# Optimization experiments

Measured on AMD Instinct MI355X. Metric: run time of the kernel, lower is better.

Reference implementation:

```python
import jax, jax.numpy as jnp
import numpy as np

N = 131072
K = 27
FIN = 3
FOUT = 32
EPS = 1e-5


def _bn(h, gamma, beta, mean, var):
    return (h - mean) * jax.lax.rsqrt(var + EPS) * gamma + beta


def setup_inputs() -> dict:
    key = jax.random.key(0)
    ks = jax.random.split(key, 8)
    return {
        "x_feats": jax.random.normal(ks[0], (N, FIN), jnp.float32),
        "z_feats": jax.random.normal(ks[1], (N, FIN), jnp.float32),
        "nbr_idx": jax.random.randint(ks[2], (N, K), 0, N, jnp.int32),
        "w1": jax.random.normal(ks[3], (K, FIN, FOUT), jnp.float32) * 0.2,
        "bn1_gamma": jnp.ones((FOUT,), jnp.float32),
        "bn1_beta": jnp.zeros((FOUT,), jnp.float32),
        "bn1_mean": jax.random.normal(ks[4], (FOUT,), jnp.float32) * 0.1,
        "bn1_var": jax.random.uniform(ks[5], (FOUT,), jnp.float32, 0.5, 1.5),
        "w2": jax.random.normal(ks[6], (K, FOUT, FOUT), jnp.float32) * 0.1,
        "mlp_w": jax.random.normal(ks[7], (FIN, FOUT), jnp.float32) * 0.3,
        "mlp_b": jnp.zeros((FOUT,), jnp.float32),
        "mlp_gamma": jnp.ones((FOUT,), jnp.float32),
        "mlp_beta": jnp.zeros((FOUT,), jnp.float32),
        "mlp_mean": jnp.zeros((FOUT,), jnp.float32),
        "mlp_var": jnp.ones((FOUT,), jnp.float32),
    }


def reference(x_feats, z_feats, nbr_idx, w1, bn1_gamma, bn1_beta, bn1_mean,
              bn1_var, w2, mlp_w, mlp_b, mlp_gamma, mlp_beta, mlp_mean,
              mlp_var):
    # --- voxel branch: sparse conv (gather-GEMM) -> BN -> SiLU -> sparse conv
    g1 = x_feats[nbr_idx]                       # [N, K, FIN] irregular gather
    h = jnp.einsum('nkf,kfo->no', g1, w1)       # [N, FOUT]
    h = jax.nn.silu(_bn(h, bn1_gamma, bn1_beta, bn1_mean, bn1_var))
    g2 = h[nbr_idx]                             # [N, K, FOUT] irregular gather
    x_out = jnp.einsum('nkf,kfo->no', g2, w2)   # [N, FOUT]

    # --- point branch: SharedMLP = Linear -> BN -> ReLU
    z = z_feats @ mlp_w + mlp_b
    z = jax.nn.relu(_bn(z, mlp_gamma, mlp_beta, mlp_mean, mlp_var))

    # --- mixed_mix: fuse voxel and point features additively
    fused = x_out + z
    return (fused, fused)
```

## Files before the change

### kernel.cpp

```cpp
#include <hip/hip_runtime.h>
#include <math.h>

#define NN 131072
#define KK 27
#define FIN 3
#define FOUT 32
#define EPS 1e-5f

typedef _Float16 f16;
typedef __attribute__((ext_vector_type(8))) _Float16 f16x8;
typedef __attribute__((ext_vector_type(16))) float f32x16;

__global__ __launch_bounds__(256) void pack_w2_kernel(
    const float* __restrict__ w2, f16* __restrict__ w2p)
{
    const int t = blockIdx.x * 256 + threadIdx.x;
    if (t >= KK * 2 * 64 * 8) return;
    const int k    = t >> 10;
    const int rem  = t & 1023;
    const int half = rem >> 9;
    const int l    = (rem >> 3) & 63;
    const int j    = rem & 7;
    const int krow = half * 16 + ((l >> 5) << 3) + j;
    const int n    = l & 31;
    w2p[t] = (f16)w2[k * (FOUT * FOUT) + krow * FOUT + n];
}

__global__ __launch_bounds__(256) void conv1_kernel(
    const float* __restrict__ x_feats,
    const int*   __restrict__ nbr_idx,
    const float* __restrict__ w1,
    const float* __restrict__ g1,  const float* __restrict__ b1,
    const float* __restrict__ m1,  const float* __restrict__ v1,
    f16* __restrict__ h_out)
{
    const int n = blockIdx.x * 256 + threadIdx.x;

    int idxs[KK];
    const int* nb = nbr_idx + (size_t)n * KK;
#pragma unroll
    for (int k = 0; k < KK; ++k) idxs[k] = nb[k];

    float acc[FOUT];
#pragma unroll
    for (int o = 0; o < FOUT; ++o) acc[o] = 0.f;

#pragma unroll
    for (int c = 0; c < 3; ++c) {
        float xs[9][3];
#pragma unroll
        for (int q = 0; q < 9; ++q) {
            const float* xr = x_feats + (size_t)idxs[c * 9 + q] * FIN;
            xs[q][0] = xr[0]; xs[q][1] = xr[1]; xs[q][2] = xr[2];
        }
#pragma unroll
        for (int q = 0; q < 9; ++q) {
            const float* w = w1 + (c * 9 + q) * (FIN * FOUT);
#pragma unroll
            for (int o = 0; o < FOUT; ++o) {
                float a = acc[o];
                a = fmaf(xs[q][0], w[o],            a);
                a = fmaf(xs[q][1], w[FOUT + o],     a);
                a = fmaf(xs[q][2], w[2 * FOUT + o], a);
                acc[o] = a;
            }
        }
    }

    f16* hr = h_out + (size_t)n * FOUT;
#pragma unroll
    for (int g = 0; g < 4; ++g) {
        f16x8 hv;
#pragma unroll
        for (int j = 0; j < 8; ++j) {
            const int o = g * 8 + j;
            const float sc = g1[o] * rsqrtf(v1[o] + EPS);
            float v = (acc[o] - m1[o]) * sc + b1[o];
            v = v / (1.f + __expf(-v));
            hv[j] = (f16)v;
        }
        *(f16x8*)(hr + g * 8) = hv;
    }
}

__global__ __launch_bounds__(256) void conv2_mfma_kernel(
    const f16*   __restrict__ h,
    const int*   __restrict__ nbr_idx,
    const f16*   __restrict__ w2p,
    const float* __restrict__ z_feats,
    const float* __restrict__ mlp_w,
    const float* __restrict__ mlp_b,
    const float* __restrict__ mg, const float* __restrict__ mbe,
    const float* __restrict__ mm, const float* __restrict__ mv,
    float* __restrict__ out)
{
    const int lane = threadIdx.x & 63;
    const int wave = threadIdx.x >> 6;
    const int base = (blockIdx.x * 4 + wave) * 32;
    const int row  = lane & 31;
    const int hi   = lane >> 5;

    int idxs[KK];
    const int* nb = nbr_idx + (size_t)(base + row) * KK;
#pragma unroll
    for (int k = 0; k < KK; ++k) idxs[k] = nb[k];

    f32x16 acc = {};

    const f16x8* bp = (const f16x8*)w2p;
#pragma unroll 3
    for (int k = 0; k < KK; ++k) {
        const f16* hr = h + (size_t)idxs[k] * FOUT + hi * 8;
        const f16x8 a1 = *(const f16x8*)hr;
        const f16x8 a2 = *(const f16x8*)(hr + 16);
        const f16x8 b1 = bp[k * 128 + lane];
        const f16x8 b2 = bp[k * 128 + 64 + lane];
        acc = __builtin_amdgcn_mfma_f32_32x32x16_f16(a1, b1, acc, 0, 0, 0);
        acc = __builtin_amdgcn_mfma_f32_32x32x16_f16(a2, b2, acc, 0, 0, 0);
    }

    const int n0 = lane & 31;
    const float wc0 = mlp_w[n0];
    const float wc1 = mlp_w[FOUT + n0];
    const float wc2 = mlp_w[2 * FOUT + n0];
    const float sc  = mg[n0] * rsqrtf(mv[n0] + EPS);
    const float bi  = mlp_b[n0];
    const float mmv = mm[n0];
    const float mbv = mbe[n0];

#pragma unroll
    for (int r = 0; r < 16; ++r) {
        const int m    = (r & 3) + ((r >> 2) << 3) + (hi << 2);
        const int node = base + m;
        const float* zr = z_feats + (size_t)node * FIN;
        float z = bi;
        z = fmaf(zr[0], wc0, z);
        z = fmaf(zr[1], wc1, z);
        z = fmaf(zr[2], wc2, z);
        z = (z - mmv) * sc + mbv;
        z = fmaxf(z, 0.f);
        const float v = acc[r] + z;
        out[(size_t)node * FOUT + n0] = v;
        out[(size_t)NN * FOUT + (size_t)node * FOUT + n0] = v;
    }
}

extern "C" void kernel_launch(void* const* d_in, const int* in_sizes, int n_in,
                              void* d_out, int out_size, void* d_ws, size_t ws_size,
                              hipStream_t stream) {
    const float* x_feats = (const float*)d_in[0];
    const float* z_feats = (const float*)d_in[1];
    const int*   nbr_idx = (const int*)d_in[2];
    const float* w1      = (const float*)d_in[3];
    const float* bn1_g   = (const float*)d_in[4];
    const float* bn1_b   = (const float*)d_in[5];
    const float* bn1_m   = (const float*)d_in[6];
    const float* bn1_v   = (const float*)d_in[7];
    const float* w2      = (const float*)d_in[8];
    const float* mlp_w   = (const float*)d_in[9];
    const float* mlp_b   = (const float*)d_in[10];
    const float* mlp_g   = (const float*)d_in[11];
    const float* mlp_be  = (const float*)d_in[12];
    const float* mlp_m   = (const float*)d_in[13];
    const float* mlp_v   = (const float*)d_in[14];

    f16* h   = (f16*)d_ws;
    f16* w2p = (f16*)((char*)d_ws + (size_t)8 * 1024 * 1024);
    float* out = (float*)d_out;

    pack_w2_kernel<<<(KK * 1024 + 255) / 256, 256, 0, stream>>>(w2, w2p);
    conv1_kernel<<<NN / 256, 256, 0, stream>>>(x_feats, nbr_idx, w1,
                                               bn1_g, bn1_b, bn1_m, bn1_v, h);
    conv2_mfma_kernel<<<NN / 128, 256, 0, stream>>>(h, nbr_idx, w2p, z_feats,
                                                    mlp_w, mlp_b, mlp_g, mlp_be,
                                                    mlp_m, mlp_v, out);
}
```

Before: 167.5 us.

## Split conv1 outputs across waves and conv2 neighbor range across wave pairs

conv1 now assigns each wave an 8-channel output slice of the same 64 nodes, so each thread keeps 8 accumulators instead of 32 and the grid has four times as many threads. conv2 splits the 27 neighbor offsets (padded to 28 with zero weights) across two waves per 32-node tile and reduces the partial MFMA accumulators through LDS. Both changes aim to raise parallelism and latency hiding for the irregular gathers. In exchange, conv1 re-gathers each node's neighbor features four times, and conv2 adds a block-wide barrier, an LDS exchange and one padded MFMA step per wave.

```diff
diff --git a/kernel.cpp b/kernel.cpp
--- a/kernel.cpp
+++ b/kernel.cpp
@@ -3,6 +3,7 @@
 
 #define NN 131072
 #define KK 27
+#define KP 28
 #define FIN 3
 #define FOUT 32
 #define EPS 1e-5f
@@ -15,7 +16,7 @@
     const float* __restrict__ w2, f16* __restrict__ w2p)
 {
     const int t = blockIdx.x * 256 + threadIdx.x;
-    if (t >= KK * 2 * 64 * 8) return;
+    if (t >= KP * 2 * 64 * 8) return;
     const int k    = t >> 10;
     const int rem  = t & 1023;
     const int half = rem >> 9;
@@ -23,7 +24,7 @@
     const int j    = rem & 7;
     const int krow = half * 16 + ((l >> 5) << 3) + j;
     const int n    = l & 31;
-    w2p[t] = (f16)w2[k * (FOUT * FOUT) + krow * FOUT + n];
+    w2p[t] = (k < KK) ? (f16)w2[k * (FOUT * FOUT) + krow * FOUT + n] : (f16)0.f;
 }
 
 __global__ __launch_bounds__(256) void conv1_kernel(
@@ -34,30 +35,32 @@
     const float* __restrict__ m1,  const float* __restrict__ v1,
     f16* __restrict__ h_out)
 {
-    const int n = blockIdx.x * 256 + threadIdx.x;
+    const int ln = threadIdx.x & 63;
+    const int n  = blockIdx.x * 64 + ln;
+    const int ob = __builtin_amdgcn_readfirstlane((threadIdx.x >> 6) * 8);
 
-    int idxs[KK];
     const int* nb = nbr_idx + (size_t)n * KK;
+
+    float acc[8];
 #pragma unroll
-    for (int k = 0; k < KK; ++k) idxs[k] = nb[k];
-
-    float acc[FOUT];
-#pragma unroll
-    for (int o = 0; o < FOUT; ++o) acc[o] = 0.f;
+    for (int o = 0; o < 8; ++o) acc[o] = 0.f;
 
 #pragma unroll
     for (int c = 0; c < 3; ++c) {
+        int idxs[9];
+#pragma unroll
+        for (int q = 0; q < 9; ++q) idxs[q] = nb[c * 9 + q];
         float xs[9][3];
 #pragma unroll
         for (int q = 0; q < 9; ++q) {
-            const float* xr = x_feats + (size_t)idxs[c * 9 + q] * FIN;
+            const float* xr = x_feats + (size_t)idxs[q] * FIN;
             xs[q][0] = xr[0]; xs[q][1] = xr[1]; xs[q][2] = xr[2];
         }
 #pragma unroll
         for (int q = 0; q < 9; ++q) {
-            const float* w = w1 + (c * 9 + q) * (FIN * FOUT);
+            const float* w = w1 + (c * 9 + q) * (FIN * FOUT) + ob;
 #pragma unroll
-            for (int o = 0; o < FOUT; ++o) {
+            for (int o = 0; o < 8; ++o) {
                 float a = acc[o];
                 a = fmaf(xs[q][0], w[o],            a);
                 a = fmaf(xs[q][1], w[FOUT + o],     a);
@@ -67,20 +70,16 @@
         }
     }
 
-    f16* hr = h_out + (size_t)n * FOUT;
+    f16x8 hv;
 #pragma unroll
-    for (int g = 0; g < 4; ++g) {
-        f16x8 hv;
-#pragma unroll
-        for (int j = 0; j < 8; ++j) {
-            const int o = g * 8 + j;
-            const float sc = g1[o] * rsqrtf(v1[o] + EPS);
-            float v = (acc[o] - m1[o]) * sc + b1[o];
-            v = v / (1.f + __expf(-v));
-            hv[j] = (f16)v;
-        }
-        *(f16x8*)(hr + g * 8) = hv;
+    for (int j = 0; j < 8; ++j) {
+        const int o = ob + j;
+        const float sc = g1[o] * rsqrtf(v1[o] + EPS);
+        float v = (acc[j] - m1[o]) * sc + b1[o];
+        v = v / (1.f + __expf(-v));
+        hv[j] = (f16)v;
     }
+    *(f16x8*)(h_out + (size_t)n * FOUT + ob) = hv;
 }
 
 __global__ __launch_bounds__(256) void conv2_mfma_kernel(
@@ -94,32 +93,42 @@
     const float* __restrict__ mm, const float* __restrict__ mv,
     float* __restrict__ out)
 {
+    __shared__ float lds[2][16][64];
+
     const int lane = threadIdx.x & 63;
-    const int wave = threadIdx.x >> 6;
-    const int base = (blockIdx.x * 4 + wave) * 32;
+    const int g    = __builtin_amdgcn_readfirstlane((threadIdx.x >> 7) & 1);
+    const int kh   = __builtin_amdgcn_readfirstlane((threadIdx.x >> 6) & 1);
+    const int base = (blockIdx.x * 2 + g) * 32;
     const int row  = lane & 31;
     const int hi   = lane >> 5;
+    const int k0   = kh * 14;
 
-    int idxs[KK];
+    int idxs[14];
     const int* nb = nbr_idx + (size_t)(base + row) * KK;
 #pragma unroll
-    for (int k = 0; k < KK; ++k) idxs[k] = nb[k];
+    for (int i = 0; i < 14; ++i)
+        idxs[i] = (k0 + i < KK) ? nb[k0 + i] : 0;
 
     f32x16 acc = {};
-
-    const f16x8* bp = (const f16x8*)w2p;
-#pragma unroll 3
-    for (int k = 0; k < KK; ++k) {
-        const f16* hr = h + (size_t)idxs[k] * FOUT + hi * 8;
+    const f16x8* bp = (const f16x8*)w2p + (size_t)k0 * 128;
+#pragma unroll 2
+    for (int i = 0; i < 14; ++i) {
+        const f16* hr = h + (size_t)idxs[i] * FOUT + hi * 8;
         const f16x8 a1 = *(const f16x8*)hr;
         const f16x8 a2 = *(const f16x8*)(hr + 16);
-        const f16x8 b1 = bp[k * 128 + lane];
-        const f16x8 b2 = bp[k * 128 + 64 + lane];
+        const f16x8 b1 = bp[i * 128 + lane];
+        const f16x8 b2 = bp[i * 128 + 64 + lane];
         acc = __builtin_amdgcn_mfma_f32_32x32x16_f16(a1, b1, acc, 0, 0, 0);
         acc = __builtin_amdgcn_mfma_f32_32x32x16_f16(a2, b2, acc, 0, 0, 0);
     }
 
-    const int n0 = lane & 31;
+    const int wr0 = kh ? 0 : 8;
+#pragma unroll
+    for (int j = 0; j < 8; ++j)
+        lds[g][wr0 + j][lane] = acc[wr0 + j];
+    __syncthreads();
+
+    const int n0  = lane & 31;
     const float wc0 = mlp_w[n0];
     const float wc1 = mlp_w[FOUT + n0];
     const float wc2 = mlp_w[2 * FOUT + n0];
@@ -128,10 +137,13 @@
     const float mmv = mm[n0];
     const float mbv = mbe[n0];
 
+    const int r0 = kh ? 8 : 0;
 #pragma unroll
-    for (int r = 0; r < 16; ++r) {
+    for (int j = 0; j < 8; ++j) {
+        const int r    = r0 + j;
         const int m    = (r & 3) + ((r >> 2) << 3) + (hi << 2);
         const int node = base + m;
+        const float v0 = acc[r] + lds[g][r][lane];
         const float* zr = z_feats + (size_t)node * FIN;
         float z = bi;
         z = fmaf(zr[0], wc0, z);
@@ -139,7 +151,7 @@
         z = fmaf(zr[2], wc2, z);
         z = (z - mmv) * sc + mbv;
         z = fmaxf(z, 0.f);
-        const float v = acc[r] + z;
+        const float v = v0 + z;
         out[(size_t)node * FOUT + n0] = v;
         out[(size_t)NN * FOUT + (size_t)node * FOUT + n0] = v;
     }
@@ -168,10 +180,10 @@
     f16* w2p = (f16*)((char*)d_ws + (size_t)8 * 1024 * 1024);
     float* out = (float*)d_out;
 
-    pack_w2_kernel<<<(KK * 1024 + 255) / 256, 256, 0, stream>>>(w2, w2p);
-    conv1_kernel<<<NN / 256, 256, 0, stream>>>(x_feats, nbr_idx, w1,
-                                               bn1_g, bn1_b, bn1_m, bn1_v, h);
-    conv2_mfma_kernel<<<NN / 128, 256, 0, stream>>>(h, nbr_idx, w2p, z_feats,
-                                                    mlp_w, mlp_b, mlp_g, mlp_be,
-                                                    mlp_m, mlp_v, out);
+    pack_w2_kernel<<<(KP * 1024 + 255) / 256, 256, 0, stream>>>(w2, w2p);
+    conv1_kernel<<<NN / 64, 256, 0, stream>>>(x_feats, nbr_idx, w1,
+                                              bn1_g, bn1_b, bn1_m, bn1_v, h);
+    conv2_mfma_kernel<<<NN / 64, 256, 0, stream>>>(h, nbr_idx, w2p, z_feats,
+                                                   mlp_w, mlp_b, mlp_g, mlp_be,
+                                                   mlp_m, mlp_v, out);
 }
```

Result: slower. 194.8 us (+16.3%).
